# Performance work log

Hardware: AMD Instinct MI355X
Metric: run time of the kernel (lower is better)

## Reference

```python
import jax, jax.numpy as jnp
import numpy as np

B, T, D = 32, 512, 240
HF, PF = 1024, 512
HB, PB = 1024, 512
BWD_BLOCK = 32
CLIP = 1.0


def setup_inputs() -> dict:
    key = jax.random.key(0)
    ks = jax.random.split(key, 8)
    u = lambda k, shape: jax.random.uniform(k, shape, jnp.float32, -0.05, 0.05)
    return {
        "data": jax.random.normal(ks[0], (B, T, D), jnp.float32),
        "mask": jnp.ones((B, T), jnp.float32),
        "weight_x_fwd": u(ks[1], (4 * HF, D)),
        "weight_r_fwd": u(ks[2], (4 * HF, PF)),
        "weight_bias_fwd": jnp.zeros((1, 4 * HF), jnp.float32),
        "weight_p_fwd": u(ks[3], (PF, HF)),
        "weight_x_bwd": u(ks[4], (4 * HB, D)),
        "weight_r_bwd": u(ks[5], (4 * HB, PB)),
        "weight_bias_bwd": jnp.zeros((1, 4 * HB), jnp.float32),
        "weight_p_bwd": u(ks[6], (PB, HB)),
    }


def _lstmp_scan(xg, wr, wp, mask, clip, hidden):
    """LSTM-with-projection scan.
    xg:   [T, N, 4H] precomputed input-side gate pre-activations (incl. bias)
    wr:   [4H, P] recurrent weights acting on projected state
    wp:   [P, H] projection weights
    mask: [T, N, 1] float mask (state held where mask==0)
    """
    N = xg.shape[1]
    P = wp.shape[0]
    c0 = jnp.zeros((N, hidden), xg.dtype)
    r0 = jnp.zeros((N, P), xg.dtype)

    def step(carry, inp):
        c, r = carry
        gx, m = inp
        gates = gx + r @ wr.T                      # [N, 4H]
        i, f, g, o = jnp.split(gates, 4, axis=-1)
        i = jax.nn.sigmoid(i)
        f = jax.nn.sigmoid(f)
        g = jnp.tanh(g)
        o = jax.nn.sigmoid(o)
        c_new = jnp.clip(f * c + i * g, -clip, clip)  # cell clipping
        r_new = (o * jnp.tanh(c_new)) @ wp.T          # project H -> P
        c = m * c_new + (1.0 - m) * c
        r = m * r_new + (1.0 - m) * r
        return (c, r), r

    _, rs = jax.lax.scan(step, (c0, r0), (xg, mask))
    return rs  # [T, N, P]


def reference(data, mask, weight_x_fwd, weight_r_fwd, weight_bias_fwd, weight_p_fwd,
              weight_x_bwd, weight_r_bwd, weight_bias_bwd, weight_p_bwd):
    Bx, Tx, _ = data.shape
    m = mask[..., None]  # [B, T, 1]

    # ---- forward direction: full left-to-right scan ----
    xg_f = jnp.einsum('btd,gd->tbg', data, weight_x_fwd) + weight_bias_fwd[0]
    m_f = jnp.swapaxes(m, 0, 1)  # [T, B, 1]
    out_f = _lstmp_scan(xg_f, weight_r_fwd, weight_p_fwd, m_f, CLIP, HF)
    out_f = jnp.swapaxes(out_f, 0, 1)  # [B, T, PF]

    # ---- backward direction: right-to-left within blocks of BWD_BLOCK ----
    L = BWD_BLOCK
    nb = Tx // L
    xg_b = jnp.einsum('btd,gd->btg', data, weight_x_bwd) + weight_bias_bwd[0]
    # split into blocks and reverse time within each block; blocks become batch
    xg_b = xg_b.reshape(Bx, nb, L, 4 * HB)[:, :, ::-1]
    xg_b = xg_b.transpose(2, 0, 1, 3).reshape(L, Bx * nb, 4 * HB)
    m_b = m.reshape(Bx, nb, L, 1)[:, :, ::-1].transpose(2, 0, 1, 3).reshape(L, Bx * nb, 1)
    out_b = _lstmp_scan(xg_b, weight_r_bwd, weight_p_bwd, m_b, CLIP, HB)
    out_b = out_b.reshape(L, Bx, nb, PB).transpose(1, 2, 0, 3)[:, :, ::-1]
    out_b = out_b.reshape(Bx, Tx, PB)

    return jnp.concatenate([out_f, out_b], axis=-1)  # [B, T, PF+PB]
```

## Files before the change

kernel.cpp:

```cpp
#include <hip/hip_runtime.h>
#include <hip/hip_bf16.h>
#include <math.h>


typedef __bf16 bf16_t;
typedef __bf16 bf16x8 __attribute__((ext_vector_type(8)));
typedef float f32x4 __attribute__((ext_vector_type(4)));
typedef unsigned int uint32;
typedef unsigned long long u64;

#define DEV __device__ __forceinline__

DEV bf16x8 ldg8(const bf16_t* p) { return *reinterpret_cast<const bf16x8*>(p); }
DEV bf16x8 ld_llc8(const bf16_t* p) {
  union { bf16x8 v; u64 q[2]; } u;
  u64* pp = (u64*)p;
  u.q[0] = __hip_atomic_load(pp, __ATOMIC_RELAXED, __HIP_MEMORY_SCOPE_AGENT);
  u.q[1] = __hip_atomic_load(pp + 1, __ATOMIC_RELAXED, __HIP_MEMORY_SCOPE_AGENT);
  return u.v;
}
DEV void st_llc_u32(uint32* p, uint32 v) {
  __hip_atomic_store(p, v, __ATOMIC_RELAXED, __HIP_MEMORY_SCOPE_AGENT);
}
DEV f32x4 mfma16(bf16x8 a, bf16x8 b, f32x4 c) {
  return __builtin_amdgcn_mfma_f32_16x16x32_bf16(a, b, c, 0, 0, 0);
}
DEV float sigmoidf_(float x) { return 1.0f / (1.0f + __expf(-x)); }
DEV float tanhf_(float x) {
  float e = __expf(2.0f * x);
  return (e - 1.0f) / (e + 1.0f);
}
DEV unsigned short bfbits(float x) {
  union { __bf16 b; unsigned short s; } u; u.b = (bf16_t)x; return u.s;
}

struct Params {
  const float* data;
  const float* mask;
  const float* wx_f; const float* wr_f; const float* bias_f; const float* wp_f;
  const float* wx_b; const float* wr_b; const float* bias_b; const float* wp_b;
  float* out;
  bf16_t* data_bf;
  bf16_t* Wf;
  bf16_t* Wb;
  bf16_t* wrf;
  bf16_t* wpT;
  bf16_t* wpf;
  bf16_t* wpb;
  float* bias_f_p;
  float* bias_b_p;
  bf16_t* h_hist;
  bf16_t* h_buf;
  bf16_t* r_buf;
  f32x4*  chb;
  int* fcnt;
  int* bcA;
  int* bcC;
};

DEV void poll_ge(int* p, int tgt) {
  while (__hip_atomic_load(p, __ATOMIC_RELAXED, __HIP_MEMORY_SCOPE_AGENT) < tgt)
    __builtin_amdgcn_s_sleep(1);
}
DEV void st_slot(int* p, int v) {
  __hip_atomic_store(p, v, __ATOMIC_RELAXED, __HIP_MEMORY_SCOPE_AGENT);
}
DEV void drain_sync() {
  asm volatile("s_waitcnt vmcnt(0)" ::: "memory");
  __syncthreads();
}

__global__ void k_data(Params P) {
  int idx = blockIdx.x * 256 + threadIdx.x;
  int k = idx & 255; int row = idx >> 8;
  float v = (k < 240) ? P.data[(size_t)row * 240 + k] : 0.0f;
  P.data_bf[idx] = (bf16_t)v;
}

__global__ void k_prep_w(Params P) {
  int idx = blockIdx.x * 256 + threadIdx.x;
  int n = 4096 * 512;
  if (idx < n) { P.wrf[idx] = (bf16_t)P.wr_f[idx]; return; }
  idx -= n; n = 1024 * 512;
  if (idx < n) { int h = idx >> 9, p = idx & 511;
                 P.wpT[idx] = (bf16_t)P.wp_f[(size_t)p * 1024 + h]; return; }
  idx -= n; n = 512 * 1024;
  if (idx < n) { P.wpf[idx] = (bf16_t)P.wp_f[idx]; return; }
  idx -= n; n = 512 * 1024;
  if (idx < n) { P.wpb[idx] = (bf16_t)P.wp_b[idx]; return; }
}

__global__ void k_packf(Params P) {
  int pr = blockIdx.x, k = threadIdx.x;
  int jj = pr >> 5, lr = pr & 31, grp = lr >> 3, uu = lr & 7;
  int grow = grp * 1024 + jj * 8 + uu;
  float v = (k < 240) ? P.wx_f[(size_t)grow * 240 + k] : 0.0f;
  P.Wf[(size_t)pr * 1280 + 1024 + k] = (bf16_t)v;
  if (k == 0) P.bias_f_p[pr] = P.bias_f[grow];
}

__global__ void k_packb(Params P) {
  int pr = blockIdx.x; int k = blockIdx.y * 256 + threadIdx.x;
  int ut = pr >> 8, rem = pr & 255, grp = rem >> 6, uu = rem & 63;
  int grow = grp * 1024 + ut * 64 + uu;
  float v;
  if (k < 512) v = P.wr_b[(size_t)grow * 512 + k];
  else { int kx = k - 512; v = (kx < 240) ? P.wx_b[(size_t)grow * 240 + kx] : 0.0f; }
  P.Wb[(size_t)pr * 768 + k] = (bf16_t)v;
  if (k == 0) P.bias_b_p[pr] = P.bias_b[grow];
}

__global__ void wc_gemm(Params P) {
  int tid = threadIdx.x, lane = tid & 63, wave = tid >> 6;
  int lane15 = lane & 15, laneh = lane >> 4;
  int mt = blockIdx.x >> 4, nt = blockIdx.x & 15;
  f32x4 acc[4] = {};
  for (int kc = 0; kc < 16; ++kc) {
    int kl = kc * 32 + laneh * 8;
    bf16x8 bv = ldg8(P.wpT + (size_t)(nt * 64 + wave * 16 + lane15) * 512 + kl);
#pragma unroll
    for (int mh = 0; mh < 4; ++mh) {
      bf16x8 av = ldg8(P.wrf + (size_t)(mt * 64 + mh * 16 + lane15) * 512 + kl);
      acc[mh] = mfma16(av, bv, acc[mh]);
    }
  }
#pragma unroll
  for (int mh = 0; mh < 4; ++mh)
#pragma unroll
    for (int q = 0; q < 4; ++q) {
      int m = mt * 64 + mh * 16 + laneh * 4 + q;
      int grp = m >> 10, unit = m & 1023, jj = unit >> 3, u8 = unit & 7;
      int pr = jj * 32 + grp * 8 + u8;
      int ncol = nt * 64 + wave * 16 + lane15;
      P.Wf[(size_t)pr * 1280 + ncol] = (bf16_t)acc[mh][q];
    }
}

__global__ void __launch_bounds__(256, 1) scan_kernel(Params P) {
  __shared__ union SM {
    float red[4][2][2][16][17];
    float gates[4][64][64];
  } sm;
  const int tid = threadIdx.x;
  const int lane = tid & 63, wave = tid >> 6;
  const int lane15 = lane & 15, laneh = lane >> 4;

  if (blockIdx.x < 128) {
    const int j = blockIdx.x;
    const bf16_t* Wfp = P.Wf + (size_t)(j * 32) * 1280;
    bf16x8 wh[2][8], wx[2][2];
#pragma unroll
    for (int nh = 0; nh < 2; ++nh) {
#pragma unroll
      for (int kc = 0; kc < 8; ++kc)
        wh[nh][kc] = ldg8(Wfp + (size_t)(nh * 16 + lane15) * 1280 +
                          wave * 256 + kc * 32 + laneh * 8);
#pragma unroll
      for (int kc = 0; kc < 2; ++kc)
        wx[nh][kc] = ldg8(Wfp + (size_t)(nh * 16 + lane15) * 1280 +
                          1024 + wave * 64 + kc * 32 + laneh * 8);
    }
    const int cb = tid >> 2, up = tid & 3;
    float biasr[2][4];
    if (tid < 128) {
#pragma unroll
      for (int e = 0; e < 2; ++e)
#pragma unroll
        for (int g = 0; g < 4; ++g)
          biasr[e][g] = P.bias_f_p[j * 32 + g * 8 + 2 * up + e];
    }
    float c_st[2] = {0.f, 0.f}, h_st[2] = {0.f, 0.f};

    for (int t = 0; t < 512; ++t) {
      f32x4 acc[2][2] = {};
      {
        bf16x8 ax[2][2];
#pragma unroll
        for (int kc = 0; kc < 2; ++kc) {
          int kx = wave * 64 + kc * 32 + laneh * 8;
          ax[0][kc] = ldg8(P.data_bf + ((size_t)(lane15 * 512 + t)) * 256 + kx);
          ax[1][kc] = ldg8(P.data_bf + ((size_t)((16 + lane15) * 512 + t)) * 256 + kx);
        }
#pragma unroll
        for (int kc = 0; kc < 2; ++kc)
#pragma unroll
          for (int m = 0; m < 2; ++m) {
            acc[m][0] = mfma16(ax[m][kc], wx[0][kc], acc[m][0]);
            acc[m][1] = mfma16(ax[m][kc], wx[1][kc], acc[m][1]);
          }
      }
      if (t > 0) {
        if (tid < 128) poll_ge(P.fcnt + tid * 16, t);
        __syncthreads();
        asm volatile("" ::: "memory");
        const bf16_t* hrow = P.h_hist + (size_t)(t - 1) * 32768;
        bf16x8 ah[2][8];
#pragma unroll
        for (int kc = 0; kc < 8; ++kc) {
          int kl = wave * 256 + kc * 32 + laneh * 8;
          ah[0][kc] = ldg8(hrow + (size_t)lane15 * 1024 + kl);
          ah[1][kc] = ldg8(hrow + (size_t)(16 + lane15) * 1024 + kl);
        }
#pragma unroll
        for (int kc = 0; kc < 8; ++kc)
#pragma unroll
          for (int m = 0; m < 2; ++m) {
            acc[m][0] = mfma16(ah[m][kc], wh[0][kc], acc[m][0]);
            acc[m][1] = mfma16(ah[m][kc], wh[1][kc], acc[m][1]);
          }
      } else {
        __syncthreads();
      }
#pragma unroll
      for (int m = 0; m < 2; ++m)
#pragma unroll
        for (int nh = 0; nh < 2; ++nh)
#pragma unroll
          for (int q = 0; q < 4; ++q)
            sm.red[wave][m][nh][laneh * 4 + q][lane15] = acc[m][nh][q];
      __syncthreads();

      if (tid < 128) {
        float mk = P.mask[cb * 512 + t];
        uint32 pk = 0;
#pragma unroll
        for (int e = 0; e < 2; ++e) {
          float g4[4];
#pragma unroll
          for (int g = 0; g < 4; ++g) {
            int lr = g * 8 + 2 * up + e;
            float v = biasr[e][g];
#pragma unroll
            for (int w2 = 0; w2 < 4; ++w2)
              v += sm.red[w2][cb >> 4][lr >> 4][cb & 15][lr & 15];
            g4[g] = v;
          }
          float iv = sigmoidf_(g4[0]);
          float fv = sigmoidf_(g4[1]);
          float gv = tanhf_(g4[2]);
          float ov = sigmoidf_(g4[3]);
          float cnew = fminf(1.0f, fmaxf(-1.0f, fv * c_st[e] + iv * gv));
          float hnew = ov * tanhf_(cnew);
          c_st[e] = mk * cnew + (1.0f - mk) * c_st[e];
          h_st[e] = mk * hnew + (1.0f - mk) * h_st[e];
          pk |= ((uint32)bfbits(h_st[e])) << (16 * e);
        }
        st_llc_u32((uint32*)(P.h_hist + (size_t)t * 32768 + cb * 1024 + j * 8 + 2 * up), pk);
      }
      drain_sync();
      if (tid == 0) st_slot(&P.fcnt[j * 16], t + 1);
    }
  } else {
    const int bx = blockIdx.x - 128;
    const int btA = bx >> 4, utA = bx & 15;
    const int btC = bx >> 3, ptC = bx & 7;
    const int un = tid & 31, nr = tid >> 5;
    float biasB[2][4];
#pragma unroll
    for (int e = 0; e < 2; ++e)
#pragma unroll
      for (int g = 0; g < 4; ++g)
        biasB[e][g] = P.bias_b_p[utA * 256 + g * 64 + 2 * un + e];

    for (int s = 0; s < 32; ++s) {
      if (s > 0) {
        if (tid < 16) {
          int bxp = (btA * 2 + (tid >> 3)) * 8 + (tid & 7);
          poll_ge(P.bcC + bxp * 16, s);
        }
        __syncthreads();
        asm volatile("" ::: "memory");
      } else {
        __syncthreads();
      }
      f32x4 acc[4][4] = {};
      const bf16_t* WbBase = P.Wb + (size_t)(utA * 256 + wave * 64) * 768;
      for (int kc = 0; kc < 24; ++kc) {
        int kb = kc * 32;
        if (kb < 512 && s == 0) continue;
        int kl = kb + laneh * 8;
        bf16x8 av[4];
        if (kb < 512) {
#pragma unroll
          for (int mh = 0; mh < 4; ++mh)
            av[mh] = ld_llc8(P.r_buf + (size_t)(btA * 64 + mh * 16 + lane15) * 512 + kl);
        } else {
          int kx = kl - 512;
#pragma unroll
          for (int mh = 0; mh < 4; ++mh) {
            int n = btA * 64 + mh * 16 + lane15;
            int t2 = (n & 15) * 32 + 31 - s;
            av[mh] = ldg8(P.data_bf + ((size_t)((n >> 4) * 512 + t2)) * 256 + kx);
          }
        }
#pragma unroll
        for (int nf = 0; nf < 4; ++nf) {
          bf16x8 bv = ldg8(WbBase + (size_t)(nf * 16 + lane15) * 768 + kl);
#pragma unroll
          for (int mh = 0; mh < 4; ++mh)
            acc[mh][nf] = mfma16(av[mh], bv, acc[mh][nf]);
        }
      }
#pragma unroll
      for (int mh = 0; mh < 4; ++mh)
#pragma unroll
        for (int nf = 0; nf < 4; ++nf)
#pragma unroll
          for (int q = 0; q < 4; ++q)
            sm.gates[wave][mh * 16 + laneh * 4 + q][nf * 16 + lane15] = acc[mh][nf][q];
      __syncthreads();

      for (int ii = 0; ii < 8; ++ii) {
        int n = ii * 8 + nr;
        int ng = btA * 64 + n;
        int b = ng >> 4;
        int t2 = (ng & 15) * 32 + 31 - s;
        float mk = P.mask[b * 512 + t2];
        size_t cix = (size_t)ng * 512 + utA * 32 + un;
        f32x4 chv;
        if (s == 0) { chv[0] = 0.f; chv[1] = 0.f; chv[2] = 0.f; chv[3] = 0.f; }
        else chv = P.chb[cix];
        uint32 pk = 0;
#pragma unroll
        for (int e = 0; e < 2; ++e) {
          float gi = sm.gates[0][n][2 * un + e] + biasB[e][0];
          float gf = sm.gates[1][n][2 * un + e] + biasB[e][1];
          float gg = sm.gates[2][n][2 * un + e] + biasB[e][2];
          float go = sm.gates[3][n][2 * un + e] + biasB[e][3];
          float iv = sigmoidf_(gi), fv = sigmoidf_(gf);
          float gv = tanhf_(gg), ov = sigmoidf_(go);
          float cold = chv[2 * e], hold = chv[2 * e + 1];
          float cnew = fminf(1.0f, fmaxf(-1.0f, fv * cold + iv * gv));
          float hnew = ov * tanhf_(cnew);
          float cm = mk * cnew + (1.0f - mk) * cold;
          float hm = mk * hnew + (1.0f - mk) * hold;
          chv[2 * e] = cm; chv[2 * e + 1] = hm;
          pk |= ((uint32)bfbits(hm)) << (16 * e);
        }
        P.chb[cix] = chv;
        st_llc_u32((uint32*)(P.h_buf + (size_t)ng * 1024 + utA * 64 + 2 * un), pk);
      }
      drain_sync();
      if (tid == 0) st_slot(&P.bcA[bx * 16], s + 1);

      if (tid < 16) poll_ge(P.bcA + ((btC >> 1) * 16 + tid) * 16, s + 1);
      __syncthreads();
      asm volatile("" ::: "memory");
      f32x4 acc2[2] = {};
      for (int kc = 0; kc < 32; ++kc) {
        int kl = kc * 32 + laneh * 8;
        bf16x8 bv = ldg8(P.wpb + (size_t)(ptC * 64 + wave * 16 + lane15) * 1024 + kl);
        bf16x8 a0 = ld_llc8(P.h_buf + (size_t)(btC * 32 + lane15) * 1024 + kl);
        bf16x8 a1 = ld_llc8(P.h_buf + (size_t)(btC * 32 + 16 + lane15) * 1024 + kl);
        acc2[0] = mfma16(a0, bv, acc2[0]);
        acc2[1] = mfma16(a1, bv, acc2[1]);
      }
#pragma unroll
      for (int mh = 0; mh < 2; ++mh)
#pragma unroll
        for (int q = 0; q < 4; ++q) {
          int nl = mh * 16 + laneh * 4 + q;
          int ng = btC * 32 + nl;
          int b = ng >> 4;
          int t2 = (ng & 15) * 32 + 31 - s;
          int p = ptC * 64 + wave * 16 + lane15;
          float v = acc2[mh][q];
          P.out[((size_t)b * 512 + t2) * 1024 + 512 + p] = v;
          float v2 = __shfl_xor(v, 1);
          if (!(lane & 1)) {
            uint32 pk = ((uint32)bfbits(v2) << 16) | bfbits(v);
            st_llc_u32((uint32*)(P.r_buf + (size_t)ng * 512 + p), pk);
          }
        }
      drain_sync();
      if (tid == 0) st_slot(&P.bcC[bx * 16], s + 1);
    }
  }
}

__global__ void fwd_proj(Params P) {
  int tid = threadIdx.x, lane = tid & 63, wave = tid >> 6;
  int lane15 = lane & 15, laneh = lane >> 4;
  int mt = blockIdx.x >> 3, nt = blockIdx.x & 7;
  f32x4 acc[4] = {};
  for (int kc = 0; kc < 32; ++kc) {
    int kl = kc * 32 + laneh * 8;
    bf16x8 bv = ldg8(P.wpf + (size_t)(nt * 64 + wave * 16 + lane15) * 1024 + kl);
#pragma unroll
    for (int mh = 0; mh < 4; ++mh) {
      bf16x8 av = ldg8(P.h_hist + (size_t)(mt * 64 + mh * 16 + lane15) * 1024 + kl);
      acc[mh] = mfma16(av, bv, acc[mh]);
    }
  }
#pragma unroll
  for (int mh = 0; mh < 4; ++mh)
#pragma unroll
    for (int q = 0; q < 4; ++q) {
      int m = mt * 64 + mh * 16 + laneh * 4 + q;
      int t = m >> 5, nb = m & 31;
      int p = nt * 64 + wave * 16 + lane15;
      P.out[((size_t)nb * 512 + t) * 1024 + p] = acc[mh][q];
    }
}

extern "C" void kernel_launch(void* const* d_in, const int* in_sizes, int n_in,
                              void* d_out, int out_size, void* d_ws, size_t ws_size,
                              hipStream_t stream) {
  (void)in_sizes; (void)n_in; (void)out_size; (void)ws_size;
  Params P;
  P.data   = (const float*)d_in[0];
  P.mask   = (const float*)d_in[1];
  P.wx_f   = (const float*)d_in[2];
  P.wr_f   = (const float*)d_in[3];
  P.bias_f = (const float*)d_in[4];
  P.wp_f   = (const float*)d_in[5];
  P.wx_b   = (const float*)d_in[6];
  P.wr_b   = (const float*)d_in[7];
  P.bias_b = (const float*)d_in[8];
  P.wp_b   = (const float*)d_in[9];
  P.out    = (float*)d_out;

  char* ws = (char*)d_ws;
  size_t o = 0;
  auto take = [&](size_t bytes) -> char* {
    char* p = ws + o; o += (bytes + 255) & ~(size_t)255; return p;
  };
  P.data_bf  = (bf16_t*)take(32ull * 512 * 256 * 2);
  P.Wf       = (bf16_t*)take(4096ull * 1280 * 2);
  P.Wb       = (bf16_t*)take(4096ull * 768 * 2);
  P.wrf      = (bf16_t*)take(4096ull * 512 * 2);
  P.wpT      = (bf16_t*)take(1024ull * 512 * 2);
  P.wpf      = (bf16_t*)take(512ull * 1024 * 2);
  P.wpb      = (bf16_t*)take(512ull * 1024 * 2);
  P.bias_f_p = (float*)take(4096 * 4);
  P.bias_b_p = (float*)take(4096 * 4);
  P.h_hist   = (bf16_t*)take(512ull * 32 * 1024 * 2);
  P.h_buf    = (bf16_t*)take(512ull * 1024 * 2);
  P.r_buf    = (bf16_t*)take(512ull * 512 * 2);
  P.chb      = (f32x4*)take(512ull * 512 * 16);
  size_t slot_i = 128ull * 16;
  char* cnts = take(3 * slot_i * 4);
  P.fcnt = (int*)cnts;
  P.bcA  = (int*)(cnts + slot_i * 4);
  P.bcC  = (int*)(cnts + 2 * slot_i * 4);

  hipMemsetAsync(cnts, 0, 3 * slot_i * 4, stream);
  k_data<<<16384, 256, 0, stream>>>(P);
  k_prep_w<<<14336, 256, 0, stream>>>(P);
  k_packf<<<4096, 256, 0, stream>>>(P);
  k_packb<<<dim3(4096, 3), 256, 0, stream>>>(P);
  wc_gemm<<<1024, 256, 0, stream>>>(P);
  scan_kernel<<<256, 256, 0, stream>>>(P);
  fwd_proj<<<2048, 256, 0, stream>>>(P);
}
```

Measured before the change: 2.510 ms.

## Replace forward-scan counter flags with sentinel-polled data in h history

Drops the per-block step counters and barrier-plus-drain handshake in the forward recurrence. Consumers now spin directly on the h_hist payload until no 64-bit word equals an all-ones sentinel. Producers pair lanes with a shuffle so each h word is written by a single 64-bit atomic store. This takes the store drain, a barrier and the flag round trip off the serial per-step critical path. In exchange it adds a large memset of the history buffer to 0xFF every call, and it relies on valid bf16 data never forming the all-ones pattern.

```diff
diff --git a/kernel.cpp b/kernel.cpp
--- a/kernel.cpp
+++ b/kernel.cpp
@@ -12,11 +12,16 @@
 #define DEV __device__ __forceinline__
 
 DEV bf16x8 ldg8(const bf16_t* p) { return *reinterpret_cast<const bf16x8*>(p); }
+DEV u64 ld_a64(const u64* p) {
+  return __hip_atomic_load(p, __ATOMIC_RELAXED, __HIP_MEMORY_SCOPE_AGENT);
+}
+DEV void st_a64(u64* p, u64 v) {
+  __hip_atomic_store(p, v, __ATOMIC_RELAXED, __HIP_MEMORY_SCOPE_AGENT);
+}
 DEV bf16x8 ld_llc8(const bf16_t* p) {
   union { bf16x8 v; u64 q[2]; } u;
   u64* pp = (u64*)p;
-  u.q[0] = __hip_atomic_load(pp, __ATOMIC_RELAXED, __HIP_MEMORY_SCOPE_AGENT);
-  u.q[1] = __hip_atomic_load(pp + 1, __ATOMIC_RELAXED, __HIP_MEMORY_SCOPE_AGENT);
+  u.q[0] = ld_a64(pp); u.q[1] = ld_a64(pp + 1);
   return u.v;
 }
 DEV void st_llc_u32(uint32* p, uint32 v) {
@@ -53,7 +58,6 @@
   bf16_t* h_buf;
   bf16_t* r_buf;
   f32x4*  chb;
-  int* fcnt;
   int* bcA;
   int* bcC;
 };
@@ -190,27 +194,36 @@
           }
       }
       if (t > 0) {
-        if (tid < 128) poll_ge(P.fcnt + tid * 16, t);
-        __syncthreads();
-        asm volatile("" ::: "memory");
         const bf16_t* hrow = P.h_hist + (size_t)(t - 1) * 32768;
-        bf16x8 ah[2][8];
-#pragma unroll
-        for (int kc = 0; kc < 8; ++kc) {
-          int kl = wave * 256 + kc * 32 + laneh * 8;
-          ah[0][kc] = ldg8(hrow + (size_t)lane15 * 1024 + kl);
-          ah[1][kc] = ldg8(hrow + (size_t)(16 + lane15) * 1024 + kl);
+        union QU { u64 q[2]; bf16x8 v; } qa[2][8];
+        for (;;) {
+          bool ok = true;
+#pragma unroll
+          for (int m = 0; m < 2; ++m)
+#pragma unroll
+            for (int kc = 0; kc < 8; ++kc) {
+              u64* p = (u64*)(hrow + (size_t)(m * 16 + lane15) * 1024 +
+                              wave * 256 + kc * 32 + laneh * 8);
+              qa[m][kc].q[0] = ld_a64(p);
+              qa[m][kc].q[1] = ld_a64(p + 1);
+            }
+#pragma unroll
+          for (int m = 0; m < 2; ++m)
+#pragma unroll
+            for (int kc = 0; kc < 8; ++kc)
+              ok = ok & (qa[m][kc].q[0] != ~0ull) & (qa[m][kc].q[1] != ~0ull);
+          if (__builtin_expect(ok, 1)) break;
+          __builtin_amdgcn_s_sleep(1);
         }
 #pragma unroll
         for (int kc = 0; kc < 8; ++kc)
 #pragma unroll
           for (int m = 0; m < 2; ++m) {
-            acc[m][0] = mfma16(ah[m][kc], wh[0][kc], acc[m][0]);
-            acc[m][1] = mfma16(ah[m][kc], wh[1][kc], acc[m][1]);
+            acc[m][0] = mfma16(qa[m][kc].v, wh[0][kc], acc[m][0]);
+            acc[m][1] = mfma16(qa[m][kc].v, wh[1][kc], acc[m][1]);
           }
-      } else {
-        __syncthreads();
-      }
+      }
+      __syncthreads();
 #pragma unroll
       for (int m = 0; m < 2; ++m)
 #pragma unroll
@@ -245,10 +258,12 @@
           h_st[e] = mk * hnew + (1.0f - mk) * h_st[e];
           pk |= ((uint32)bfbits(h_st[e])) << (16 * e);
         }
-        st_llc_u32((uint32*)(P.h_hist + (size_t)t * 32768 + cb * 1024 + j * 8 + 2 * up), pk);
-      }
-      drain_sync();
-      if (tid == 0) st_slot(&P.fcnt[j * 16], t + 1);
+        uint32 po = __shfl_xor((int)pk, 1);
+        if (!(up & 1)) {
+          u64 qq = (u64)pk | ((u64)po << 32);
+          st_a64((u64*)(P.h_hist + (size_t)t * 32768 + cb * 1024 + j * 8 + 2 * up), qq);
+        }
+      }
     }
   } else {
     const int bx = blockIdx.x - 128;
@@ -439,12 +454,12 @@
   P.r_buf    = (bf16_t*)take(512ull * 512 * 2);
   P.chb      = (f32x4*)take(512ull * 512 * 16);
   size_t slot_i = 128ull * 16;
-  char* cnts = take(3 * slot_i * 4);
-  P.fcnt = (int*)cnts;
-  P.bcA  = (int*)(cnts + slot_i * 4);
-  P.bcC  = (int*)(cnts + 2 * slot_i * 4);
-
-  hipMemsetAsync(cnts, 0, 3 * slot_i * 4, stream);
+  char* cnts = take(2 * slot_i * 4);
+  P.bcA  = (int*)cnts;
+  P.bcC  = (int*)(cnts + slot_i * 4);
+
+  hipMemsetAsync(cnts, 0, 2 * slot_i * 4, stream);
+  hipMemsetAsync(P.h_hist, 0xFF, 512ull * 32 * 1024 * 2, stream);
   k_data<<<16384, 256, 0, stream>>>(P);
   k_prep_w<<<14336, 256, 0, stream>>>(P);
   k_packf<<<4096, 256, 0, stream>>>(P);
```

Result: slower. 4.589 ms (+82.8%).

## Split forward-scan work by full-K per wave and remove LDS reduction

Applied to the files above, without the earlier changes.

The forward recurrent block now gives each wave a 16x16 output tile over the full K range (recurrent plus input weights kept in 40 register fragments), instead of splitting K across waves. This removes the shared-memory cross-wave reduction and one __syncthreads per timestep. Gate rows are repacked so that i/f/g/o for a unit sit in adjacent columns and can be gathered with lane shuffles. Hidden outputs are packed via shuffles into 64-bit stores. The change raises register pressure and adds shuffle overhead.

```diff
diff --git a/kernel.cpp b/kernel.cpp
--- a/kernel.cpp
+++ b/kernel.cpp
@@ -12,11 +12,16 @@
 #define DEV __device__ __forceinline__
 
 DEV bf16x8 ldg8(const bf16_t* p) { return *reinterpret_cast<const bf16x8*>(p); }
+DEV u64 ld_a64(const u64* p) {
+  return __hip_atomic_load(p, __ATOMIC_RELAXED, __HIP_MEMORY_SCOPE_AGENT);
+}
+DEV void st_a64(u64* p, u64 v) {
+  __hip_atomic_store(p, v, __ATOMIC_RELAXED, __HIP_MEMORY_SCOPE_AGENT);
+}
 DEV bf16x8 ld_llc8(const bf16_t* p) {
   union { bf16x8 v; u64 q[2]; } u;
   u64* pp = (u64*)p;
-  u.q[0] = __hip_atomic_load(pp, __ATOMIC_RELAXED, __HIP_MEMORY_SCOPE_AGENT);
-  u.q[1] = __hip_atomic_load(pp + 1, __ATOMIC_RELAXED, __HIP_MEMORY_SCOPE_AGENT);
+  u.q[0] = ld_a64(pp); u.q[1] = ld_a64(pp + 1);
   return u.v;
 }
 DEV void st_llc_u32(uint32* p, uint32 v) {
@@ -32,6 +37,12 @@
 }
 DEV unsigned short bfbits(float x) {
   union { __bf16 b; unsigned short s; } u; u.b = (bf16_t)x; return u.s;
+}
+DEV f32x4 shfl_xor4(f32x4 v, int m) {
+  f32x4 r;
+  r[0] = __shfl_xor(v[0], m); r[1] = __shfl_xor(v[1], m);
+  r[2] = __shfl_xor(v[2], m); r[3] = __shfl_xor(v[3], m);
+  return r;
 }
 
 struct Params {
@@ -92,8 +103,8 @@
 
 __global__ void k_packf(Params P) {
   int pr = blockIdx.x, k = threadIdx.x;
-  int jj = pr >> 5, lr = pr & 31, grp = lr >> 3, uu = lr & 7;
-  int grow = grp * 1024 + jj * 8 + uu;
+  int j = pr >> 5, q = pr & 31, nh = q >> 4, u4 = (q >> 2) & 3, g = q & 3;
+  int grow = g * 1024 + j * 8 + nh * 4 + u4;
   float v = (k < 240) ? P.wx_f[(size_t)grow * 240 + k] : 0.0f;
   P.Wf[(size_t)pr * 1280 + 1024 + k] = (bf16_t)v;
   if (k == 0) P.bias_f_p[pr] = P.bias_f[grow];
@@ -129,123 +140,107 @@
 #pragma unroll
     for (int q = 0; q < 4; ++q) {
       int m = mt * 64 + mh * 16 + laneh * 4 + q;
-      int grp = m >> 10, unit = m & 1023, jj = unit >> 3, u8 = unit & 7;
-      int pr = jj * 32 + grp * 8 + u8;
+      int grp = m >> 10, unit = m & 1023;
+      int j = unit >> 3, rem = unit & 7, nh = rem >> 2, u4 = rem & 3;
+      int pr = j * 32 + nh * 16 + u4 * 4 + grp;
       int ncol = nt * 64 + wave * 16 + lane15;
       P.Wf[(size_t)pr * 1280 + ncol] = (bf16_t)acc[mh][q];
     }
 }
 
 __global__ void __launch_bounds__(256, 1) scan_kernel(Params P) {
-  __shared__ union SM {
-    float red[4][2][2][16][17];
-    float gates[4][64][64];
-  } sm;
+  __shared__ float gates_sm[4][64][64];
   const int tid = threadIdx.x;
   const int lane = tid & 63, wave = tid >> 6;
   const int lane15 = lane & 15, laneh = lane >> 4;
 
   if (blockIdx.x < 128) {
     const int j = blockIdx.x;
-    const bf16_t* Wfp = P.Wf + (size_t)(j * 32) * 1280;
-    bf16x8 wh[2][8], wx[2][2];
-#pragma unroll
-    for (int nh = 0; nh < 2; ++nh) {
-#pragma unroll
-      for (int kc = 0; kc < 8; ++kc)
-        wh[nh][kc] = ldg8(Wfp + (size_t)(nh * 16 + lane15) * 1280 +
-                          wave * 256 + kc * 32 + laneh * 8);
-#pragma unroll
-      for (int kc = 0; kc < 2; ++kc)
-        wx[nh][kc] = ldg8(Wfp + (size_t)(nh * 16 + lane15) * 1280 +
-                          1024 + wave * 64 + kc * 32 + laneh * 8);
-    }
-    const int cb = tid >> 2, up = tid & 3;
-    float biasr[2][4];
-    if (tid < 128) {
-#pragma unroll
-      for (int e = 0; e < 2; ++e)
-#pragma unroll
-        for (int g = 0; g < 4; ++g)
-          biasr[e][g] = P.bias_f_p[j * 32 + g * 8 + 2 * up + e];
-    }
-    float c_st[2] = {0.f, 0.f}, h_st[2] = {0.f, 0.f};
+    const int mh = wave & 1, nh = wave >> 1;
+    const int col = lane15;
+    const int g = col & 3, u4 = col >> 2;
+    const bf16_t* Wfp = P.Wf + (size_t)(j * 32 + nh * 16 + col) * 1280;
+    bf16x8 wb[40];
+#pragma unroll
+    for (int kc = 0; kc < 40; ++kc)
+      wb[kc] = ldg8(Wfp + kc * 32 + laneh * 8);
+    const float biasv = P.bias_f_p[j * 32 + nh * 16 + col];
+    float c_st[4] = {0.f, 0.f, 0.f, 0.f}, h_st[4] = {0.f, 0.f, 0.f, 0.f};
+    const int brow = mh * 16 + lane15;
+    const int bq0 = mh * 16 + laneh * 4;
 
     for (int t = 0; t < 512; ++t) {
-      f32x4 acc[2][2] = {};
+      float mk[4];
+#pragma unroll
+      for (int q = 0; q < 4; ++q) mk[q] = P.mask[(bq0 + q) * 512 + t];
+      f32x4 a0 = {biasv, biasv, biasv, biasv};
+      f32x4 a1 = {}, a2 = {}, a3 = {};
       {
-        bf16x8 ax[2][2];
-#pragma unroll
-        for (int kc = 0; kc < 2; ++kc) {
-          int kx = wave * 64 + kc * 32 + laneh * 8;
-          ax[0][kc] = ldg8(P.data_bf + ((size_t)(lane15 * 512 + t)) * 256 + kx);
-          ax[1][kc] = ldg8(P.data_bf + ((size_t)((16 + lane15) * 512 + t)) * 256 + kx);
-        }
-#pragma unroll
-        for (int kc = 0; kc < 2; ++kc)
-#pragma unroll
-          for (int m = 0; m < 2; ++m) {
-            acc[m][0] = mfma16(ax[m][kc], wx[0][kc], acc[m][0]);
-            acc[m][1] = mfma16(ax[m][kc], wx[1][kc], acc[m][1]);
-          }
+        const bf16_t* xrow = P.data_bf + ((size_t)brow * 512 + t) * 256 + laneh * 8;
+        bf16x8 ax[8];
+#pragma unroll
+        for (int kk = 0; kk < 8; ++kk) ax[kk] = ldg8(xrow + kk * 32);
+        a0 = mfma16(ax[0], wb[32], a0); a1 = mfma16(ax[1], wb[33], a1);
+        a2 = mfma16(ax[2], wb[34], a2); a3 = mfma16(ax[3], wb[35], a3);
+        a0 = mfma16(ax[4], wb[36], a0); a1 = mfma16(ax[5], wb[37], a1);
+        a2 = mfma16(ax[6], wb[38], a2); a3 = mfma16(ax[7], wb[39], a3);
       }
       if (t > 0) {
         if (tid < 128) poll_ge(P.fcnt + tid * 16, t);
         __syncthreads();
         asm volatile("" ::: "memory");
-        const bf16_t* hrow = P.h_hist + (size_t)(t - 1) * 32768;
-        bf16x8 ah[2][8];
-#pragma unroll
-        for (int kc = 0; kc < 8; ++kc) {
-          int kl = wave * 256 + kc * 32 + laneh * 8;
-          ah[0][kc] = ldg8(hrow + (size_t)lane15 * 1024 + kl);
-          ah[1][kc] = ldg8(hrow + (size_t)(16 + lane15) * 1024 + kl);
-        }
-#pragma unroll
-        for (int kc = 0; kc < 8; ++kc)
-#pragma unroll
-          for (int m = 0; m < 2; ++m) {
-            acc[m][0] = mfma16(ah[m][kc], wh[0][kc], acc[m][0]);
-            acc[m][1] = mfma16(ah[m][kc], wh[1][kc], acc[m][1]);
-          }
+        const bf16_t* hrow = P.h_hist + (size_t)(t - 1) * 32768 +
+                             (size_t)brow * 1024 + laneh * 8;
+#pragma unroll
+        for (int c8 = 0; c8 < 4; ++c8) {
+          bf16x8 ah[8];
+#pragma unroll
+          for (int kk = 0; kk < 8; ++kk) ah[kk] = ldg8(hrow + c8 * 256 + kk * 32);
+          a0 = mfma16(ah[0], wb[c8 * 8 + 0], a0);
+          a1 = mfma16(ah[1], wb[c8 * 8 + 1], a1);
+          a2 = mfma16(ah[2], wb[c8 * 8 + 2], a2);
+          a3 = mfma16(ah[3], wb[c8 * 8 + 3], a3);
+          a0 = mfma16(ah[4], wb[c8 * 8 + 4], a0);
+          a1 = mfma16(ah[5], wb[c8 * 8 + 5], a1);
+          a2 = mfma16(ah[6], wb[c8 * 8 + 6], a2);
+          a3 = mfma16(ah[7], wb[c8 * 8 + 7], a3);
+        }
       } else {
         __syncthreads();
       }
-#pragma unroll
-      for (int m = 0; m < 2; ++m)
-#pragma unroll
-        for (int nh = 0; nh < 2; ++nh)
-#pragma unroll
-          for (int q = 0; q < 4; ++q)
-            sm.red[wave][m][nh][laneh * 4 + q][lane15] = acc[m][nh][q];
-      __syncthreads();
-
-      if (tid < 128) {
-        float mk = P.mask[cb * 512 + t];
-        uint32 pk = 0;
-#pragma unroll
-        for (int e = 0; e < 2; ++e) {
-          float g4[4];
-#pragma unroll
-          for (int g = 0; g < 4; ++g) {
-            int lr = g * 8 + 2 * up + e;
-            float v = biasr[e][g];
-#pragma unroll
-            for (int w2 = 0; w2 < 4; ++w2)
-              v += sm.red[w2][cb >> 4][lr >> 4][cb & 15][lr & 15];
-            g4[g] = v;
-          }
-          float iv = sigmoidf_(g4[0]);
-          float fv = sigmoidf_(g4[1]);
-          float gv = tanhf_(g4[2]);
-          float ov = sigmoidf_(g4[3]);
-          float cnew = fminf(1.0f, fmaxf(-1.0f, fv * c_st[e] + iv * gv));
-          float hnew = ov * tanhf_(cnew);
-          c_st[e] = mk * cnew + (1.0f - mk) * c_st[e];
-          h_st[e] = mk * hnew + (1.0f - mk) * h_st[e];
-          pk |= ((uint32)bfbits(h_st[e])) << (16 * e);
-        }
-        st_llc_u32((uint32*)(P.h_hist + (size_t)t * 32768 + cb * 1024 + j * 8 + 2 * up), pk);
+      f32x4 vacc = (a0 + a1) + (a2 + a3);
+      f32x4 v1 = shfl_xor4(vacc, 1);
+      f32x4 lo = (g & 1) ? v1 : vacc;
+      f32x4 hi = (g & 1) ? vacc : v1;
+      f32x4 lo2 = shfl_xor4(lo, 2);
+      f32x4 hi2 = shfl_xor4(hi, 2);
+      f32x4 gi_ = (g & 2) ? lo2 : lo;
+      f32x4 gf_ = (g & 2) ? hi2 : hi;
+      f32x4 gg_ = (g & 2) ? lo : lo2;
+      f32x4 go_ = (g & 2) ? hi : hi2;
+      uint32 hb[4];
+#pragma unroll
+      for (int q = 0; q < 4; ++q) {
+        float iv = sigmoidf_(gi_[q]);
+        float fv = sigmoidf_(gf_[q]);
+        float gv = tanhf_(gg_[q]);
+        float ov = sigmoidf_(go_[q]);
+        float cnew = fminf(1.0f, fmaxf(-1.0f, fv * c_st[q] + iv * gv));
+        float hnew = ov * tanhf_(cnew);
+        c_st[q] = mk[q] * cnew + (1.0f - mk[q]) * c_st[q];
+        h_st[q] = mk[q] * hnew + (1.0f - mk[q]) * h_st[q];
+        hb[q] = bfbits(h_st[q]);
+      }
+#pragma unroll
+      for (int q = 0; q < 4; ++q) {
+        uint32 a = hb[q];
+        uint32 b1 = (uint32)__shfl_xor((int)a, 4);
+        uint32 pp = (u4 & 1) ? (b1 | (a << 16)) : (a | (b1 << 16));
+        uint32 c1 = (uint32)__shfl_xor((int)pp, 8);
+        u64 gq = (u4 & 2) ? (((u64)pp << 32) | c1) : (((u64)c1 << 32) | pp);
+        if (col == 0)
+          st_a64((u64*)(P.h_hist + (size_t)t * 32768 +
+                        (size_t)(bq0 + q) * 1024 + j * 8 + nh * 4), gq);
       }
       drain_sync();
       if (tid == 0) st_slot(&P.fcnt[j * 16], t + 1);
@@ -259,8 +254,8 @@
 #pragma unroll
     for (int e = 0; e < 2; ++e)
 #pragma unroll
-      for (int g = 0; g < 4; ++g)
-        biasB[e][g] = P.bias_b_p[utA * 256 + g * 64 + 2 * un + e];
+      for (int g2 = 0; g2 < 4; ++g2)
+        biasB[e][g2] = P.bias_b_p[utA * 256 + g2 * 64 + 2 * un + e];
 
     for (int s = 0; s < 32; ++s) {
       if (s > 0) {
@@ -282,32 +277,32 @@
         bf16x8 av[4];
         if (kb < 512) {
 #pragma unroll
-          for (int mh = 0; mh < 4; ++mh)
-            av[mh] = ld_llc8(P.r_buf + (size_t)(btA * 64 + mh * 16 + lane15) * 512 + kl);
+          for (int mh2 = 0; mh2 < 4; ++mh2)
+            av[mh2] = ld_llc8(P.r_buf + (size_t)(btA * 64 + mh2 * 16 + lane15) * 512 + kl);
         } else {
           int kx = kl - 512;
 #pragma unroll
-          for (int mh = 0; mh < 4; ++mh) {
-            int n = btA * 64 + mh * 16 + lane15;
+          for (int mh2 = 0; mh2 < 4; ++mh2) {
+            int n = btA * 64 + mh2 * 16 + lane15;
             int t2 = (n & 15) * 32 + 31 - s;
-            av[mh] = ldg8(P.data_bf + ((size_t)((n >> 4) * 512 + t2)) * 256 + kx);
+            av[mh2] = ldg8(P.data_bf + ((size_t)((n >> 4) * 512 + t2)) * 256 + kx);
           }
         }
 #pragma unroll
         for (int nf = 0; nf < 4; ++nf) {
           bf16x8 bv = ldg8(WbBase + (size_t)(nf * 16 + lane15) * 768 + kl);
 #pragma unroll
-          for (int mh = 0; mh < 4; ++mh)
-            acc[mh][nf] = mfma16(av[mh], bv, acc[mh][nf]);
-        }
-      }
-#pragma unroll
-      for (int mh = 0; mh < 4; ++mh)
+          for (int mh2 = 0; mh2 < 4; ++mh2)
+            acc[mh2][nf] = mfma16(av[mh2], bv, acc[mh2][nf]);
+        }
+      }
+#pragma unroll
+      for (int mh2 = 0; mh2 < 4; ++mh2)
 #pragma unroll
         for (int nf = 0; nf < 4; ++nf)
 #pragma unroll
           for (int q = 0; q < 4; ++q)
-            sm.gates[wave][mh * 16 + laneh * 4 + q][nf * 16 + lane15] = acc[mh][nf][q];
+            gates_sm[wave][mh2 * 16 + laneh * 4 + q][nf * 16 + lane15] = acc[mh2][nf][q];
       __syncthreads();
 
       for (int ii = 0; ii < 8; ++ii) {
@@ -323,10 +318,10 @@
         uint32 pk = 0;
 #pragma unroll
         for (int e = 0; e < 2; ++e) {
-          float gi = sm.gates[0][n][2 * un + e] + biasB[e][0];
-          float gf = sm.gates[1][n][2 * un + e] + biasB[e][1];
-          float gg = sm.gates[2][n][2 * un + e] + biasB[e][2];
-          float go = sm.gates[3][n][2 * un + e] + biasB[e][3];
+          float gi = gates_sm[0][n][2 * un + e] + biasB[e][0];
+          float gf = gates_sm[1][n][2 * un + e] + biasB[e][1];
+          float gg = gates_sm[2][n][2 * un + e] + biasB[e][2];
+          float go = gates_sm[3][n][2 * un + e] + biasB[e][3];
           float iv = sigmoidf_(gi), fv = sigmoidf_(gf);
           float gv = tanhf_(gg), ov = sigmoidf_(go);
           float cold = chv[2 * e], hold = chv[2 * e + 1];
@@ -350,21 +345,21 @@
       for (int kc = 0; kc < 32; ++kc) {
         int kl = kc * 32 + laneh * 8;
         bf16x8 bv = ldg8(P.wpb + (size_t)(ptC * 64 + wave * 16 + lane15) * 1024 + kl);
-        bf16x8 a0 = ld_llc8(P.h_buf + (size_t)(btC * 32 + lane15) * 1024 + kl);
-        bf16x8 a1 = ld_llc8(P.h_buf + (size_t)(btC * 32 + 16 + lane15) * 1024 + kl);
-        acc2[0] = mfma16(a0, bv, acc2[0]);
-        acc2[1] = mfma16(a1, bv, acc2[1]);
-      }
-#pragma unroll
-      for (int mh = 0; mh < 2; ++mh)
+        bf16x8 q0 = ld_llc8(P.h_buf + (size_t)(btC * 32 + lane15) * 1024 + kl);
+        bf16x8 q1 = ld_llc8(P.h_buf + (size_t)(btC * 32 + 16 + lane15) * 1024 + kl);
+        acc2[0] = mfma16(q0, bv, acc2[0]);
+        acc2[1] = mfma16(q1, bv, acc2[1]);
+      }
+#pragma unroll
+      for (int mh2 = 0; mh2 < 2; ++mh2)
 #pragma unroll
         for (int q = 0; q < 4; ++q) {
-          int nl = mh * 16 + laneh * 4 + q;
+          int nl = mh2 * 16 + laneh * 4 + q;
           int ng = btC * 32 + nl;
           int b = ng >> 4;
           int t2 = (ng & 15) * 32 + 31 - s;
           int p = ptC * 64 + wave * 16 + lane15;
-          float v = acc2[mh][q];
+          float v = acc2[mh2][q];
           P.out[((size_t)b * 512 + t2) * 1024 + 512 + p] = v;
           float v2 = __shfl_xor(v, 1);
           if (!(lane & 1)) {
```

New measurement: 4.303 ms. 71.4% more time.
